# Kernel optimization log

Hardware: AMD Instinct MI355X
Metric: run time of the kernel (lower is better)

## Reference

```python
import jax, jax.numpy as jnp
import numpy as np

NUM_HEADS = 16
HEAD_DIM = 64
HIDDEN = NUM_HEADS * HEAD_DIM


def _rope_tables(seq_len, dim, dtype):
    # inv_freq: [dim/2]; emb = cat(freqs, freqs): [S, dim]
    inv_freq = 1.0 / (10000.0 ** (jnp.arange(0, dim, 2, dtype=jnp.float32) / dim))
    t = jnp.arange(seq_len, dtype=jnp.float32)
    freqs = jnp.einsum('i,j->ij', t, inv_freq)
    emb = jnp.concatenate([freqs, freqs], axis=-1)
    return jnp.cos(emb).astype(dtype), jnp.sin(emb).astype(dtype)  # [S, dim] each


def _rotate_half(x):
    x1, x2 = jnp.split(x, 2, axis=-1)
    return jnp.concatenate([-x2, x1], axis=-1)


def setup_inputs() -> dict:
    key = jax.random.key(0)
    k1, k2, k3, k4 = jax.random.split(key, 4)
    B, S = 2, 2048
    hidden_states = jax.random.normal(k1, (B, S, HIDDEN), dtype=jnp.float32)
    scale = 0.02
    Wq = jax.random.normal(k2, (HIDDEN, HIDDEN), dtype=jnp.float32) * scale
    Wk = jax.random.normal(k3, (HIDDEN, HIDDEN), dtype=jnp.float32) * scale
    Wv = jax.random.normal(k4, (HIDDEN, HIDDEN), dtype=jnp.float32) * scale
    return {"hidden_states": hidden_states, "Wq": Wq, "Wk": Wk, "Wv": Wv}


def reference(hidden_states, Wq, Wk, Wv):
    B, S, H = hidden_states.shape
    # nn.Linear: x @ W.T ; reshape to [B, heads, S, head_dim]
    def split_heads(x):
        return x.reshape(B, S, NUM_HEADS, HEAD_DIM).transpose(0, 2, 1, 3)
    q = split_heads(hidden_states @ Wq.T)
    k = split_heads(hidden_states @ Wk.T)
    v = split_heads(hidden_states @ Wv.T)
    # inline RoPE over full head_dim
    cos, sin = _rope_tables(S, HEAD_DIM, q.dtype)  # [S, head_dim]
    cos = cos[None, None]  # [1,1,S,head_dim]
    sin = sin[None, None]
    q = q * cos + _rotate_half(q) * sin
    k = k * cos + _rotate_half(k) * sin
    # manual softmax attention
    scores = jnp.einsum('bhqd,bhkd->bhqk', q, k) / (HEAD_DIM ** 0.5)
    probs = jax.nn.softmax(scores, axis=-1)
    ctx = jnp.einsum('bhqk,bhkd->bhqd', probs, v)
    ctx = ctx.transpose(0, 2, 1, 3).reshape(B, S, H)
    return ctx
```

## Files before the change

kernel.cpp:

```cpp
#include <hip/hip_runtime.h>
#include <math.h>

#define NHEADS 16
#define HDIM   64
#define HID    1024
#define BATCH  2
#define SEQ    2048
#define NX (BATCH*SEQ*HID)
#define NW (HID*HID)

typedef unsigned short u16;
typedef __attribute__((ext_vector_type(8))) short  bf16x8;
typedef __attribute__((ext_vector_type(8))) unsigned short u16x8;
typedef __attribute__((ext_vector_type(4))) float  f32x4;


__device__ __forceinline__ void split8(const float* xf, bf16x8& hi, bf16x8& lo) {
    unsigned* hp = (unsigned*)&hi;
    unsigned* lp = (unsigned*)&lo;
#pragma unroll
    for (int j = 0; j < 4; j++) {
        const float p0 = xf[2 * j], p1 = xf[2 * j + 1];
        const unsigned u0 = __float_as_uint(p0);
        const unsigned u1 = __float_as_uint(p1);
        hp[j] = __builtin_amdgcn_perm(u1, u0, 0x07060302u);
        const float l0 = p0 - __uint_as_float(u0 & 0xFFFF0000u);
        const float l1 = p1 - __uint_as_float(u1 & 0xFFFF0000u);
        lp[j] = __builtin_amdgcn_perm(__float_as_uint(l1), __float_as_uint(l0), 0x07060302u);
    }
}
__device__ __forceinline__ void split1(float v, u16& h, u16& l) {
    unsigned u = __float_as_uint(v);
    h = (u16)(u >> 16);
    l = (u16)(__float_as_uint(v - __uint_as_float(u & 0xFFFF0000u)) >> 16);
}

__global__ void rope_tables_kernel(float* __restrict__ ct, float* __restrict__ st) {
    int idx = blockIdx.x * 256 + threadIdx.x;
    if (idx >= SEQ * HDIM) return;
    int s  = idx >> 6;
    int dh = idx & 63;
    int i  = dh & 31;
    float inv = exp2f(-(float)i * (13.28771237954945f / 32.0f));
    float fr  = (float)s * inv;
    ct[idx] = cosf(fr);
    st[idx] = sinf(fr);
}

__global__ __launch_bounds__(256) void split_kernel(
    const float* __restrict__ X,
    const float* __restrict__ W0,
    const float* __restrict__ W1,
    const float* __restrict__ W2,
    u16* __restrict__ Xhi, u16* __restrict__ Xlo,
    u16* __restrict__ Whi, u16* __restrict__ Wlo)
{
    const int s = blockIdx.x * 4 + (threadIdx.x >> 6);
    const int l = threadIdx.x & 63;
    const int r = l & 15, q = l >> 4;
    const float* src; u16* dh; u16* dl; int so;
    if (s < 8192) { src = X; dh = Xhi; dl = Xlo; so = s; }
    else {
        const int wi = (s - 8192) >> 11;
        so = (s - 8192) & 2047;
        src = (wi == 0) ? W0 : ((wi == 1) ? W1 : W2);
        dh = Whi + (size_t)wi * NW;
        dl = Wlo + (size_t)wi * NW;
    }
    const int R0 = (so >> 5) << 4, K0 = (so & 31) << 5;
    const float* sp = src + (size_t)(R0 + r) * 1024 + K0 + q * 8;
    float v[8];
    *(float4*)&v[0] = *(const float4*)sp;
    *(float4*)&v[4] = *(const float4*)(sp + 4);
    u16x8 h8, l8;
#pragma unroll
    for (int e = 0; e < 8; e++) {
        u16 hh, ll;
        split1(v[e], hh, ll);
        h8[e] = hh; l8[e] = ll;
    }
    const size_t off = (size_t)so * 512 + l * 8;
    *(u16x8*)(dh + off) = h8;
    *(u16x8*)(dl + off) = l8;
}

__global__ __launch_bounds__(256, 2) void qkv_mfma_kernel(
    const u16* __restrict__ Xhi, const u16* __restrict__ Xlo,
    const u16* __restrict__ Whi, const u16* __restrict__ Wlo,
    const float* __restrict__ ct, const float* __restrict__ st,
    u16* __restrict__ Qhi, u16* __restrict__ Qlo,
    u16* __restrict__ Khi, u16* __restrict__ Klo,
    u16* __restrict__ Vhi, u16* __restrict__ Vlo)
{
    __shared__ unsigned vtr[64][129];

    const int t    = threadIdx.x;
    const int lane = t & 63;
    const int w    = t >> 6;
    const int lx   = lane & 15;
    const int quad = lane >> 4;

    const int lid  = blockIdx.x;
    const int xcd  = lid & 7;
    const int i_   = lid >> 3;
    const int proj = i_ % 3;
    const int mb   = i_ / 3;
    const int nb   = xcd;
    const int n0   = nb * 128;
    const int m0   = mb * 128;

    const u16* __restrict__ Wph = Whi + (size_t)proj * NW;
    const u16* __restrict__ Wpl = Wlo + (size_t)proj * NW;

    const int am = (w & 1) * 64;
    const int bn = (w >> 1) * 64;
    const int lp = quad * 128 + lx * 8;

    const u16 *pAh[4], *pAl[4], *pBh[4], *pBl[4];
#pragma unroll
    for (int i = 0; i < 4; i++) {
        const size_t o = ((size_t)(((m0 + am) >> 4) + i) * 32) * 512 + lp;
        pAh[i] = Xhi + o; pAl[i] = Xlo + o;
    }
#pragma unroll
    for (int j = 0; j < 4; j++) {
        const size_t o = ((size_t)(((n0 + bn) >> 4) + j) * 32) * 512 + lp;
        pBh[j] = Wph + o; pBl[j] = Wpl + o;
    }

    f32x4 acc[4][4];
#pragma unroll
    for (int i = 0; i < 4; i++)
#pragma unroll
        for (int j = 0; j < 4; j++) acc[i][j] = (f32x4){0.f, 0.f, 0.f, 0.f};

    bf16x8 cah[4], cal[4], cbh[4], cbl[4];
    bf16x8 nah[4], nal[4], nbh[4], nbl[4];
#pragma unroll
    for (int i = 0; i < 4; i++) { cah[i] = *(const bf16x8*)(pAh[i]); cal[i] = *(const bf16x8*)(pAl[i]); }
#pragma unroll
    for (int j = 0; j < 4; j++) { cbh[j] = *(const bf16x8*)(pBh[j]); cbl[j] = *(const bf16x8*)(pBl[j]); }

#pragma unroll 1
    for (int kt = 0; kt < HID; kt += 64) {
        const int ko1 = ((kt + 32) >> 5) * 512;
        const int ko2 = (kt + 64 < HID) ? ((kt + 64) >> 5) * 512 : 0;

#pragma unroll
        for (int i = 0; i < 4; i++) { nah[i] = *(const bf16x8*)(pAh[i] + ko1); nal[i] = *(const bf16x8*)(pAl[i] + ko1); }
#pragma unroll
        for (int j = 0; j < 4; j++) { nbh[j] = *(const bf16x8*)(pBh[j] + ko1); nbl[j] = *(const bf16x8*)(pBl[j] + ko1); }

        __builtin_amdgcn_s_setprio(1);
#pragma unroll
        for (int j = 0; j < 4; j++)
#pragma unroll
            for (int i = 0; i < 4; i++) {
                acc[i][j] = __builtin_amdgcn_mfma_f32_16x16x32_bf16(cah[i], cbh[j], acc[i][j], 0, 0, 0);
                acc[i][j] = __builtin_amdgcn_mfma_f32_16x16x32_bf16(cal[i], cbh[j], acc[i][j], 0, 0, 0);
                acc[i][j] = __builtin_amdgcn_mfma_f32_16x16x32_bf16(cah[i], cbl[j], acc[i][j], 0, 0, 0);
            }
        __builtin_amdgcn_s_setprio(0);

#pragma unroll
        for (int i = 0; i < 4; i++) { cah[i] = *(const bf16x8*)(pAh[i] + ko2); cal[i] = *(const bf16x8*)(pAl[i] + ko2); }
#pragma unroll
        for (int j = 0; j < 4; j++) { cbh[j] = *(const bf16x8*)(pBh[j] + ko2); cbl[j] = *(const bf16x8*)(pBl[j] + ko2); }

        __builtin_amdgcn_s_setprio(1);
#pragma unroll
        for (int j = 0; j < 4; j++)
#pragma unroll
            for (int i = 0; i < 4; i++) {
                acc[i][j] = __builtin_amdgcn_mfma_f32_16x16x32_bf16(nah[i], nbh[j], acc[i][j], 0, 0, 0);
                acc[i][j] = __builtin_amdgcn_mfma_f32_16x16x32_bf16(nal[i], nbh[j], acc[i][j], 0, 0, 0);
                acc[i][j] = __builtin_amdgcn_mfma_f32_16x16x32_bf16(nah[i], nbl[j], acc[i][j], 0, 0, 0);
            }
        __builtin_amdgcn_s_setprio(0);
    }

    const int b      = m0 >> 11;
    const int head   = (n0 >> 6) + (w >> 1);
    const int m_base = m0 + am;

    if (proj < 2) {
#pragma unroll
        for (int i = 0; i < 4; i++) {
#pragma unroll
            for (int r = 0; r < 4; r++) {
                const int s = (m_base + i * 16 + quad * 4 + r) & 2047;
                const float* ctr = ct + s * HDIM;
                const float* str = st + s * HDIM;
                float nv[4];
#pragma unroll
                for (int j = 0; j < 4; j++) {
                    const int dh = j * 16 + lx;
                    const float c  = ctr[dh];
                    const float sn = str[dh];
                    const float x  = acc[i][j][r];
                    const float p  = acc[i][j ^ 2][r];
                    nv[j] = (j < 2) ? (x * c - p * sn) : (x * c + p * sn);
                }
#pragma unroll
                for (int j = 0; j < 4; j++) acc[i][j][r] = nv[j];
            }
        }
        u16* dh_ = (proj == 0) ? Qhi : Khi;
        u16* dl_ = (proj == 0) ? Qlo : Klo;
        const float qscale = (proj == 0) ? 0.18033688011112042f : 1.0f;
        const size_t obase = (size_t)(b * NHEADS + head) * SEQ * HDIM;
#pragma unroll
        for (int i = 0; i < 4; i++)
#pragma unroll
            for (int r = 0; r < 4; r++) {
                const int s   = (m_base + i * 16 + quad * 4 + r) & 2047;
                const int rb  = s >> 4;
                const int lxq = s & 15;
#pragma unroll
                for (int j = 0; j < 4; j++) {
                    const size_t fo = obase + ((size_t)rb * 2 + (j >> 1)) * 512
                                    + (size_t)((j & 1) * 2 + (lx >> 3)) * 128
                                    + (size_t)lxq * 8 + (lx & 7);
                    u16 hh, ll;
                    split1(acc[i][j][r] * qscale, hh, ll);
                    dh_[fo] = hh;
                    dl_[fo] = ll;
                }
            }
    } else {
#pragma unroll 1
        for (int pass = 0; pass < 2; pass++) {
            __syncthreads();
            if ((w & 1) == pass) {
#pragma unroll
                for (int i = 0; i < 4; i++)
#pragma unroll
                    for (int j = 0; j < 4; j++)
#pragma unroll
                        for (int r = 0; r < 4; r++) {
                            const int ml = i * 16 + quad * 4 + r;
                            const int nl = bn + j * 16 + lx;
                            const float v = acc[i][j][r];
                            unsigned u  = __float_as_uint(v);
                            unsigned hi = u & 0xFFFF0000u;
                            unsigned lo = __float_as_uint(v - __uint_as_float(hi)) >> 16;
                            vtr[ml][nl] = hi | lo;
                        }
            }
            __syncthreads();
            {
                const int d      = t >> 1;
                const int sh     = (t & 1) * 32;
                const int headv  = (n0 >> 6) + (d >> 6);
                const int dd     = d & 63;
                const size_t vbase = (size_t)(b * NHEADS + headv) * SEQ * HDIM;
                const int s0base = (m0 & 2047) + pass * 64 + sh;
#pragma unroll
                for (int k = 0; k < 4; k++) {
                    const int s0 = s0base + k * 8;
                    u16x8 hv, lv;
#pragma unroll
                    for (int e = 0; e < 8; e++) {
                        unsigned u = vtr[sh + k * 8 + e][d];
                        hv[e] = (u16)(u >> 16);
                        lv[e] = (u16)(u & 0xFFFFu);
                    }
                    const size_t fo = vbase + ((size_t)(dd >> 4) * 64 + (s0 >> 5)) * 512
                                    + (size_t)((s0 >> 3) & 3) * 128 + (size_t)(dd & 15) * 8;
                    *(u16x8*)(Vhi + fo) = hv;
                    *(u16x8*)(Vlo + fo) = lv;
                }
            }
        }
    }
}

__global__ __launch_bounds__(256, 2) void attn_kernel(
    const u16* __restrict__ Qhi, const u16* __restrict__ Qlo,
    const u16* __restrict__ Khi, const u16* __restrict__ Klo,
    const u16* __restrict__ Vhi, const u16* __restrict__ Vlo,
    float* __restrict__ OUT)
{
    __shared__ __align__(16) u16 KVs[3][4096];
    __shared__ float PS[4][32][68];

    const int t    = threadIdx.x;
    const int lane = t & 63;
    const int w    = t >> 6;
    const int lx   = lane & 15;
    const int quad = lane >> 4;

    const int q0 = blockIdx.x * 128;
    const int h  = blockIdx.y;
    const int b  = blockIdx.z;
    const size_t base = (size_t)(b * NHEADS + h) * SEQ * HDIM;
    const int lp = quad * 128 + lx * 8;

    bf16x8 qh[2][2], ql[2][2];
#pragma unroll
    for (int a = 0; a < 2; a++)
#pragma unroll
        for (int ks = 0; ks < 2; ks++) {
            const size_t fo = base + ((size_t)((q0 >> 4) + w * 2 + a) * 2 + ks) * 512 + lp;
            qh[a][ks] = *(const bf16x8*)(Qhi + fo);
            ql[a][ks] = *(const bf16x8*)(Qlo + fo);
        }

    f32x4 O[2][4];
    float l_part[2][4];
#pragma unroll
    for (int a = 0; a < 2; a++) {
#pragma unroll
        for (int dt = 0; dt < 4; dt++) O[a][dt] = (f32x4){0.f,0.f,0.f,0.f};
#pragma unroll
        for (int r = 0; r < 4; r++) l_part[a][r] = 0.f;
    }

    u16x8 sreg[6];
    auto stage_load = [&](int kt) {
#pragma unroll
        for (int i = 0; i < 6; i++) {
            const int o = (((i & 1) << 8) + t) * 8;
            const u16* g;
            if (i < 2)      g = Khi + base + (size_t)(kt >> 4) * 1024 + o;
            else if (i < 4) g = Klo + base + (size_t)(kt >> 4) * 1024 + o;
            else {
                const int dt = o >> 10, rem = o & 1023;
                g = Vhi + base + ((size_t)dt * 64 + (kt >> 5)) * 512 + rem;
            }
            sreg[i] = *(const u16x8*)g;
        }
    };

    stage_load(0);

#pragma unroll 1
    for (int kt = 0; kt < SEQ; kt += 64) {
        __syncthreads();
#pragma unroll
        for (int i = 0; i < 6; i++) {
            const int o = (((i & 1) << 8) + t) * 8;
            *(u16x8*)&KVs[i >> 1][o] = sreg[i];
        }
        __syncthreads();

        stage_load((kt + 64) & (SEQ - 1));

        bf16x8 vl[2][4];
#pragma unroll
        for (int dt = 0; dt < 4; dt++)
#pragma unroll
            for (int ks2 = 0; ks2 < 2; ks2++)
                vl[ks2][dt] = *(const bf16x8*)(Vlo + base + ((size_t)dt * 64 + (kt >> 5) + ks2) * 512 + lp);

        bf16x8 kh[2][4], kl[2][4];
#pragma unroll
        for (int c = 0; c < 4; c++)
#pragma unroll
            for (int ks = 0; ks < 2; ks++) {
                kh[ks][c] = *(const bf16x8*)&KVs[0][(c * 2 + ks) * 512 + lp];
                kl[ks][c] = *(const bf16x8*)&KVs[1][(c * 2 + ks) * 512 + lp];
            }

#pragma unroll
        for (int a = 0; a < 2; a++) {
#pragma unroll
            for (int c = 0; c < 4; c++) {
                f32x4 acc = (f32x4){0.f,0.f,0.f,0.f};
                __builtin_amdgcn_s_setprio(1);
#pragma unroll
                for (int ks = 0; ks < 2; ks++) {
                    acc = __builtin_amdgcn_mfma_f32_16x16x32_bf16(qh[a][ks], kh[ks][c], acc, 0, 0, 0);
                    acc = __builtin_amdgcn_mfma_f32_16x16x32_bf16(ql[a][ks], kh[ks][c], acc, 0, 0, 0);
                    acc = __builtin_amdgcn_mfma_f32_16x16x32_bf16(qh[a][ks], kl[ks][c], acc, 0, 0, 0);
                }
                __builtin_amdgcn_s_setprio(0);
#pragma unroll
                for (int r = 0; r < 4; r++) {
                    float p = exp2f(acc[r]);
                    l_part[a][r] += p;
                    PS[w][a * 16 + quad * 4 + r][c * 16 + lx] = p;
                }
            }
        }

        bf16x8 vh[2][4];
#pragma unroll
        for (int dt = 0; dt < 4; dt++)
#pragma unroll
            for (int ks2 = 0; ks2 < 2; ks2++)
                vh[ks2][dt] = *(const bf16x8*)&KVs[2][dt * 1024 + ks2 * 512 + lp];

#pragma unroll
        for (int a = 0; a < 2; a++) {
#pragma unroll
            for (int ks2 = 0; ks2 < 2; ks2++) {
                const float* ps = &PS[w][a * 16 + lx][ks2 * 32 + quad * 8];
                float pf[8];
                *(float4*)&pf[0] = *(const float4*)ps;
                *(float4*)&pf[4] = *(const float4*)(ps + 4);
                bf16x8 phi, plo;
                split8(pf, phi, plo);
                __builtin_amdgcn_s_setprio(1);
#pragma unroll
                for (int dt = 0; dt < 4; dt++) {
                    O[a][dt] = __builtin_amdgcn_mfma_f32_16x16x32_bf16(phi, vh[ks2][dt], O[a][dt], 0, 0, 0);
                    O[a][dt] = __builtin_amdgcn_mfma_f32_16x16x32_bf16(plo, vh[ks2][dt], O[a][dt], 0, 0, 0);
                    O[a][dt] = __builtin_amdgcn_mfma_f32_16x16x32_bf16(phi, vl[ks2][dt], O[a][dt], 0, 0, 0);
                }
                __builtin_amdgcn_s_setprio(0);
            }
        }
    }

    float linv[2][4];
#pragma unroll
    for (int a = 0; a < 2; a++)
#pragma unroll
        for (int r = 0; r < 4; r++) {
            float l = l_part[a][r];
            l += __shfl_xor(l, 1);
            l += __shfl_xor(l, 2);
            l += __shfl_xor(l, 4);
            l += __shfl_xor(l, 8);
            linv[a][r] = 1.f / l;
        }

    float* Po = &PS[0][0][0];
    __syncthreads();
#pragma unroll
    for (int a = 0; a < 2; a++)
#pragma unroll
        for (int dt = 0; dt < 4; dt++)
#pragma unroll
            for (int r = 0; r < 4; r++)
                Po[(size_t)(w * 32 + a * 16 + quad * 4 + r) * 68 + dt * 16 + lx] =
                    O[a][dt][r] * linv[a][r];
    __syncthreads();
    {
        const int q    = t >> 1;
        const int half = t & 1;
        const float* prow = Po + (size_t)q * 68 + half * 32;
        float* dst = OUT + ((size_t)(b * SEQ + q0 + q)) * HID + h * HDIM + half * 32;
#pragma unroll
        for (int e = 0; e < 8; e++)
            ((float4*)dst)[e] = ((const float4*)prow)[e];
    }
}

extern "C" void kernel_launch(void* const* d_in, const int* in_sizes, int n_in,
                              void* d_out, int out_size, void* d_ws, size_t ws_size,
                              hipStream_t stream)
{
    const float* X  = (const float*)d_in[0];
    const float* Wq = (const float*)d_in[1];
    const float* Wk = (const float*)d_in[2];
    const float* Wv = (const float*)d_in[3];
    float* out = (float*)d_out;

    const size_t qkv_elems = (size_t)BATCH * NHEADS * SEQ * HDIM;
    char* wsb = (char*)d_ws;
    float* ct  = (float*)wsb;
    float* st  = ct + (size_t)SEQ * HDIM;
    u16* Xhi = (u16*)(st + (size_t)SEQ * HDIM);
    u16* Xlo = Xhi + (size_t)NX;
    u16* Whi = Xlo + (size_t)NX;
    u16* Wlo = Whi + 3 * (size_t)NW;
    u16* Qhi = Wlo + 3 * (size_t)NW;
    u16* Qlo = Qhi + qkv_elems;
    u16* Khi = Qlo + qkv_elems;
    u16* Klo = Khi + qkv_elems;
    u16* Vhi = Klo + qkv_elems;
    u16* Vlo = Vhi + qkv_elems;

    rope_tables_kernel<<<(SEQ * HDIM + 255) / 256, 256, 0, stream>>>(ct, st);

    split_kernel<<<3584, 256, 0, stream>>>(
        X, Wq, Wk, Wv, Xhi, Xlo, Whi, Wlo);

    qkv_mfma_kernel<<<dim3(3 * (HID / 128) * ((BATCH * SEQ) / 128)), 256, 0, stream>>>(
        Xhi, Xlo, Whi, Wlo, ct, st, Qhi, Qlo, Khi, Klo, Vhi, Vlo);

    attn_kernel<<<dim3(SEQ / 128, NHEADS, BATCH), 256, 0, stream>>>(
        Qhi, Qlo, Khi, Klo, Vhi, Vlo, out);
}
```

Before: 268.2 us.

## Use 8 waves of 16 query rows each in attention kernel

The attention block grows from 256 to 512 threads. Each wave now owns 16 query rows instead of 32, which halves the per-thread Q, O and softmax-sum register state. The K/V staging load is spread over twice as many threads, so each thread carries three vectors instead of six. The aim is lower register pressure and more waves in flight to hide memory and exp latency. The cost is that each wave reuses every K/V fragment read from shared memory for fewer rows, so LDS and global Vlo reads per unit of work double.

```diff
diff --git a/kernel.cpp b/kernel.cpp
--- a/kernel.cpp
+++ b/kernel.cpp
@@ -275,14 +275,14 @@
     }
 }
 
-__global__ __launch_bounds__(256, 2) void attn_kernel(
+__global__ __launch_bounds__(512, 4) void attn_kernel(
     const u16* __restrict__ Qhi, const u16* __restrict__ Qlo,
     const u16* __restrict__ Khi, const u16* __restrict__ Klo,
     const u16* __restrict__ Vhi, const u16* __restrict__ Vlo,
     float* __restrict__ OUT)
 {
     __shared__ __align__(16) u16 KVs[3][4096];
-    __shared__ float PS[4][32][68];
+    __shared__ float PS[8][16][68];
 
     const int t    = threadIdx.x;
     const int lane = t & 63;
@@ -296,40 +296,28 @@
     const size_t base = (size_t)(b * NHEADS + h) * SEQ * HDIM;
     const int lp = quad * 128 + lx * 8;
 
-    bf16x8 qh[2][2], ql[2][2];
-#pragma unroll
-    for (int a = 0; a < 2; a++)
-#pragma unroll
-        for (int ks = 0; ks < 2; ks++) {
-            const size_t fo = base + ((size_t)((q0 >> 4) + w * 2 + a) * 2 + ks) * 512 + lp;
-            qh[a][ks] = *(const bf16x8*)(Qhi + fo);
-            ql[a][ks] = *(const bf16x8*)(Qlo + fo);
-        }
-
-    f32x4 O[2][4];
-    float l_part[2][4];
-#pragma unroll
-    for (int a = 0; a < 2; a++) {
-#pragma unroll
-        for (int dt = 0; dt < 4; dt++) O[a][dt] = (f32x4){0.f,0.f,0.f,0.f};
-#pragma unroll
-        for (int r = 0; r < 4; r++) l_part[a][r] = 0.f;
-    }
-
-    u16x8 sreg[6];
+    bf16x8 qh[2], ql[2];
+#pragma unroll
+    for (int ks = 0; ks < 2; ks++) {
+        const size_t fo = base + ((size_t)((q0 >> 4) + w) * 2 + ks) * 512 + lp;
+        qh[ks] = *(const bf16x8*)(Qhi + fo);
+        ql[ks] = *(const bf16x8*)(Qlo + fo);
+    }
+
+    f32x4 O[4];
+    float l_part[4];
+#pragma unroll
+    for (int dt = 0; dt < 4; dt++) O[dt] = (f32x4){0.f,0.f,0.f,0.f};
+#pragma unroll
+    for (int r = 0; r < 4; r++) l_part[r] = 0.f;
+
+    u16x8 sreg[3];
     auto stage_load = [&](int kt) {
-#pragma unroll
-        for (int i = 0; i < 6; i++) {
-            const int o = (((i & 1) << 8) + t) * 8;
-            const u16* g;
-            if (i < 2)      g = Khi + base + (size_t)(kt >> 4) * 1024 + o;
-            else if (i < 4) g = Klo + base + (size_t)(kt >> 4) * 1024 + o;
-            else {
-                const int dt = o >> 10, rem = o & 1023;
-                g = Vhi + base + ((size_t)dt * 64 + (kt >> 5)) * 512 + rem;
-            }
-            sreg[i] = *(const u16x8*)g;
-        }
+        const int o = t * 8;
+        sreg[0] = *(const u16x8*)(Khi + base + (size_t)(kt >> 4) * 1024 + o);
+        sreg[1] = *(const u16x8*)(Klo + base + (size_t)(kt >> 4) * 1024 + o);
+        const int dt = o >> 10, rem = o & 1023;
+        sreg[2] = *(const u16x8*)(Vhi + base + ((size_t)dt * 64 + (kt >> 5)) * 512 + rem);
     };
 
     stage_load(0);
@@ -337,10 +325,11 @@
 #pragma unroll 1
     for (int kt = 0; kt < SEQ; kt += 64) {
         __syncthreads();
-#pragma unroll
-        for (int i = 0; i < 6; i++) {
-            const int o = (((i & 1) << 8) + t) * 8;
-            *(u16x8*)&KVs[i >> 1][o] = sreg[i];
+        {
+            const int o = t * 8;
+            *(u16x8*)&KVs[0][o] = sreg[0];
+            *(u16x8*)&KVs[1][o] = sreg[1];
+            *(u16x8*)&KVs[2][o] = sreg[2];
         }
         __syncthreads();
 
@@ -363,24 +352,21 @@
             }
 
 #pragma unroll
-        for (int a = 0; a < 2; a++) {
-#pragma unroll
-            for (int c = 0; c < 4; c++) {
-                f32x4 acc = (f32x4){0.f,0.f,0.f,0.f};
-                __builtin_amdgcn_s_setprio(1);
-#pragma unroll
-                for (int ks = 0; ks < 2; ks++) {
-                    acc = __builtin_amdgcn_mfma_f32_16x16x32_bf16(qh[a][ks], kh[ks][c], acc, 0, 0, 0);
-                    acc = __builtin_amdgcn_mfma_f32_16x16x32_bf16(ql[a][ks], kh[ks][c], acc, 0, 0, 0);
-                    acc = __builtin_amdgcn_mfma_f32_16x16x32_bf16(qh[a][ks], kl[ks][c], acc, 0, 0, 0);
-                }
-                __builtin_amdgcn_s_setprio(0);
-#pragma unroll
-                for (int r = 0; r < 4; r++) {
-                    float p = exp2f(acc[r]);
-                    l_part[a][r] += p;
-                    PS[w][a * 16 + quad * 4 + r][c * 16 + lx] = p;
-                }
+        for (int c = 0; c < 4; c++) {
+            f32x4 acc = (f32x4){0.f,0.f,0.f,0.f};
+            __builtin_amdgcn_s_setprio(1);
+#pragma unroll
+            for (int ks = 0; ks < 2; ks++) {
+                acc = __builtin_amdgcn_mfma_f32_16x16x32_bf16(qh[ks], kh[ks][c], acc, 0, 0, 0);
+                acc = __builtin_amdgcn_mfma_f32_16x16x32_bf16(ql[ks], kh[ks][c], acc, 0, 0, 0);
+                acc = __builtin_amdgcn_mfma_f32_16x16x32_bf16(qh[ks], kl[ks][c], acc, 0, 0, 0);
+            }
+            __builtin_amdgcn_s_setprio(0);
+#pragma unroll
+            for (int r = 0; r < 4; r++) {
+                float p = exp2f(acc[r]);
+                l_part[r] += p;
+                PS[w][quad * 4 + r][c * 16 + lx] = p;
             }
         }
 
@@ -392,58 +378,51 @@
                 vh[ks2][dt] = *(const bf16x8*)&KVs[2][dt * 1024 + ks2 * 512 + lp];
 
 #pragma unroll
-        for (int a = 0; a < 2; a++) {
-#pragma unroll
-            for (int ks2 = 0; ks2 < 2; ks2++) {
-                const float* ps = &PS[w][a * 16 + lx][ks2 * 32 + quad * 8];
-                float pf[8];
-                *(float4*)&pf[0] = *(const float4*)ps;
-                *(float4*)&pf[4] = *(const float4*)(ps + 4);
-                bf16x8 phi, plo;
-                split8(pf, phi, plo);
-                __builtin_amdgcn_s_setprio(1);
-#pragma unroll
-                for (int dt = 0; dt < 4; dt++) {
-                    O[a][dt] = __builtin_amdgcn_mfma_f32_16x16x32_bf16(phi, vh[ks2][dt], O[a][dt], 0, 0, 0);
-                    O[a][dt] = __builtin_amdgcn_mfma_f32_16x16x32_bf16(plo, vh[ks2][dt], O[a][dt], 0, 0, 0);
-                    O[a][dt] = __builtin_amdgcn_mfma_f32_16x16x32_bf16(phi, vl[ks2][dt], O[a][dt], 0, 0, 0);
-                }
-                __builtin_amdgcn_s_setprio(0);
-            }
+        for (int ks2 = 0; ks2 < 2; ks2++) {
+            const float* ps = &PS[w][lx][ks2 * 32 + quad * 8];
+            float pf[8];
+            *(float4*)&pf[0] = *(const float4*)ps;
+            *(float4*)&pf[4] = *(const float4*)(ps + 4);
+            bf16x8 phi, plo;
+            split8(pf, phi, plo);
+            __builtin_amdgcn_s_setprio(1);
+#pragma unroll
+            for (int dt = 0; dt < 4; dt++) {
+                O[dt] = __builtin_amdgcn_mfma_f32_16x16x32_bf16(phi, vh[ks2][dt], O[dt], 0, 0, 0);
+                O[dt] = __builtin_amdgcn_mfma_f32_16x16x32_bf16(plo, vh[ks2][dt], O[dt], 0, 0, 0);
+                O[dt] = __builtin_amdgcn_mfma_f32_16x16x32_bf16(phi, vl[ks2][dt], O[dt], 0, 0, 0);
+            }
+            __builtin_amdgcn_s_setprio(0);
         }
     }
 
-    float linv[2][4];
-#pragma unroll
-    for (int a = 0; a < 2; a++)
-#pragma unroll
-        for (int r = 0; r < 4; r++) {
-            float l = l_part[a][r];
-            l += __shfl_xor(l, 1);
-            l += __shfl_xor(l, 2);
-            l += __shfl_xor(l, 4);
-            l += __shfl_xor(l, 8);
-            linv[a][r] = 1.f / l;
-        }
+    float linv[4];
+#pragma unroll
+    for (int r = 0; r < 4; r++) {
+        float l = l_part[r];
+        l += __shfl_xor(l, 1);
+        l += __shfl_xor(l, 2);
+        l += __shfl_xor(l, 4);
+        l += __shfl_xor(l, 8);
+        linv[r] = 1.f / l;
+    }
 
     float* Po = &PS[0][0][0];
     __syncthreads();
 #pragma unroll
-    for (int a = 0; a < 2; a++)
-#pragma unroll
-        for (int dt = 0; dt < 4; dt++)
-#pragma unroll
-            for (int r = 0; r < 4; r++)
-                Po[(size_t)(w * 32 + a * 16 + quad * 4 + r) * 68 + dt * 16 + lx] =
-                    O[a][dt][r] * linv[a][r];
+    for (int dt = 0; dt < 4; dt++)
+#pragma unroll
+        for (int r = 0; r < 4; r++)
+            Po[(size_t)(w * 16 + quad * 4 + r) * 68 + dt * 16 + lx] =
+                O[dt][r] * linv[r];
     __syncthreads();
     {
-        const int q    = t >> 1;
-        const int half = t & 1;
-        const float* prow = Po + (size_t)q * 68 + half * 32;
-        float* dst = OUT + ((size_t)(b * SEQ + q0 + q)) * HID + h * HDIM + half * 32;
-#pragma unroll
-        for (int e = 0; e < 8; e++)
+        const int q    = t >> 2;
+        const int part = t & 3;
+        const float* prow = Po + (size_t)q * 68 + part * 16;
+        float* dst = OUT + ((size_t)(b * SEQ + q0 + q)) * HID + h * HDIM + part * 16;
+#pragma unroll
+        for (int e = 0; e < 4; e++)
             ((float4*)dst)[e] = ((const float4*)prow)[e];
     }
 }
@@ -481,6 +460,6 @@
     qkv_mfma_kernel<<<dim3(3 * (HID / 128) * ((BATCH * SEQ) / 128)), 256, 0, stream>>>(
         Xhi, Xlo, Whi, Wlo, ct, st, Qhi, Qlo, Khi, Klo, Vhi, Vlo);
 
-    attn_kernel<<<dim3(SEQ / 128, NHEADS, BATCH), 256, 0, stream>>>(
+    attn_kernel<<<dim3(SEQ / 128, NHEADS, BATCH), 512, 0, stream>>>(
         Qhi, Qlo, Khi, Klo, Vhi, Vlo, out);
 }
```

Result: slower. 501.8 us (+87.1%).
